# Kernel tuning notes

Hardware: AMD Instinct MI355X
Metric: run time of the kernel (lower is better)

The kernel has to match this reference:

```python
import jax, jax.numpy as jnp
import numpy as np

B, N, DIM = 16, 1024, 512
H, KD, D = 16, 32, 128          # num_heads, key_dim, d = attn_ratio*key_dim
DH = H * D                      # 2048
HQKV = DH + 2 * H * KD          # 3072
RES = 32
SCALE = KD ** -0.5
EPS = 1e-5


def _make_bias_idxs():
    ii = np.arange(N)
    px, py = ii // RES, ii % RES
    dx = np.abs(px[:, None] - px[None, :])
    dy = np.abs(py[:, None] - py[None, :])
    return (dx * RES + dy).astype(np.int32)  # (N, N), values in [0, RES*RES)


def setup_inputs() -> dict:
    key = jax.random.key(0)
    ks = jax.random.split(key, 6)
    return {
        "x": jax.random.normal(ks[0], (B, N, DIM), jnp.float32),
        "gamma": jnp.ones((DIM,), jnp.float32),
        "beta": jnp.zeros((DIM,), jnp.float32),
        "qkv_w": jax.random.normal(ks[1], (HQKV, DIM), jnp.float32) * 0.02,
        "qkv_b": jax.random.normal(ks[2], (HQKV,), jnp.float32) * 0.02,
        "proj_w": jax.random.normal(ks[3], (DIM, DH), jnp.float32) * 0.02,
        "proj_b": jax.random.normal(ks[4], (DIM,), jnp.float32) * 0.02,
        "attention_biases": jax.random.normal(ks[5], (H, RES * RES), jnp.float32) * 0.02,
        "bias_idxs": jnp.asarray(_make_bias_idxs()),
    }


def reference(x, gamma, beta, qkv_w, qkv_b, proj_w, proj_b, attention_biases, bias_idxs):
    # LayerNorm
    mu = jnp.mean(x, axis=-1, keepdims=True)
    var = jnp.mean(jnp.square(x - mu), axis=-1, keepdims=True)
    xn = (x - mu) * jax.lax.rsqrt(var + EPS) * gamma + beta
    # QKV projection -> (B, H, N, kd+kd+d)
    qkv = (xn @ qkv_w.T + qkv_b).reshape(B, N, H, 2 * KD + D).transpose(0, 2, 1, 3)
    q, k, v = qkv[..., :KD], qkv[..., KD:2 * KD], qkv[..., 2 * KD:]
    # Relative-position bias gather: (H, N, N)
    bias = attention_biases[:, bias_idxs]
    attn = jnp.einsum("bhnk,bhmk->bhnm", q, k) * SCALE + bias
    attn = jax.nn.softmax(attn, axis=-1)
    out = jnp.einsum("bhnm,bhmd->bhnd", attn, v)  # (B, H, N, D)
    out = out.transpose(0, 2, 1, 3).reshape(B, N, DH)
    return out @ proj_w.T + proj_b
```

## Files before the change

### kernel.cpp

```cpp
#include <hip/hip_runtime.h>

#define DIM_   512
#define NSEQ   1024
#define BB     16
#define HH     16
#define KD_    32
#define DD_    128
#define LDQKV  3072
#define DH_    2048
#define SCALE_ 0.17677669529663687f

typedef __bf16 bf16x8 __attribute__((ext_vector_type(8)));
typedef float  f32x4  __attribute__((ext_vector_type(4)));
typedef unsigned int u32x4v __attribute__((ext_vector_type(4)));

typedef __attribute__((address_space(1))) const unsigned int guint;
typedef __attribute__((address_space(3))) unsigned int luint;
#define GLL16(gp, lp) __builtin_amdgcn_global_load_lds((guint*)(gp), (luint*)(lp), 16, 0, 0)

static __device__ __forceinline__ unsigned short f2bf(float f) {
  unsigned int u = __builtin_bit_cast(unsigned int, f);
  u += 0x7fffu + ((u >> 16) & 1u);
  return (unsigned short)(u >> 16);
}
#define SGM(t) ((((t) & 3) << 1) | (((t) >> 2) & 1))

__global__ __launch_bounds__(256) void cvt_kernel(const float* __restrict__ in,
                                                  unsigned short* __restrict__ out,
                                                  int n) {
  int i = blockIdx.x * 256 + threadIdx.x;
  if (i < n) out[i] = f2bf(in[i]);
}

__global__ __launch_bounds__(256) void ln_kernel(const float* __restrict__ x,
                                                 const float* __restrict__ gamma,
                                                 const float* __restrict__ beta,
                                                 unsigned short* __restrict__ xn) {
  int row = blockIdx.x, t = threadIdx.x;
  const float* xr = x + (size_t)row * DIM_;
  float2 v = *(const float2*)(xr + t * 2);
  float s = v.x + v.y, sq = v.x * v.x + v.y * v.y;
#pragma unroll
  for (int off = 32; off; off >>= 1) {
    s  += __shfl_xor(s, off, 64);
    sq += __shfl_xor(sq, off, 64);
  }
  __shared__ float red[8];
  int wid = t >> 6, lane = t & 63;
  if (lane == 0) { red[wid * 2] = s; red[wid * 2 + 1] = sq; }
  __syncthreads();
  float S  = red[0] + red[2] + red[4] + red[6];
  float SQ = red[1] + red[3] + red[5] + red[7];
  float mu   = S * (1.f / DIM_);
  float var  = SQ * (1.f / DIM_) - mu * mu;
  float rstd = rsqrtf(var + 1e-5f);
  int c = t * 2;
  xn[(size_t)row * DIM_ + c]     = f2bf((v.x - mu) * rstd * gamma[c]     + beta[c]);
  xn[(size_t)row * DIM_ + c + 1] = f2bf((v.y - mu) * rstd * gamma[c + 1] + beta[c + 1]);
}

template <typename OUT>
__global__ __launch_bounds__(256) void gemm_gll(const unsigned short* __restrict__ A, int lda,
                                                const unsigned short* __restrict__ W, int ldb,
                                                const float* __restrict__ bias,
                                                OUT* __restrict__ C, int ldc,
                                                int K) {
  __shared__ unsigned short a_sm[128][64];
  __shared__ unsigned short b_sm[128][64];
  int tid = threadIdx.x;
  int lane = tid & 63, w = tid >> 6;
  int quad = lane >> 4, l15 = lane & 15;
  int wr = w >> 1, wc = w & 1;
  long tm = (long)blockIdx.y * 128, tn = (long)blockIdx.x * 128;
  int srow = w * 8 + (lane >> 3), scol = (lane & 7) * 8;

  f32x4 acc[4][4] = {};

  for (int k0 = 0; k0 < K; k0 += 64) {
    __syncthreads();
#pragma unroll
    for (int it = 0; it < 4; it++) {
      GLL16(A + (tm + it * 32 + srow) * lda + k0 + scol, &a_sm[it * 32 + w * 8][0]);
      GLL16(W + (tn + it * 32 + srow) * ldb + k0 + scol, &b_sm[it * 32 + w * 8][0]);
    }
    __syncthreads();
#pragma unroll
    for (int kk = 0; kk < 64; kk += 32) {
      bf16x8 af[4], bfr[4];
#pragma unroll
      for (int i = 0; i < 4; i++)
        af[i] = *(const bf16x8*)&a_sm[wr * 64 + i * 16 + l15][kk + quad * 8];
#pragma unroll
      for (int j = 0; j < 4; j++)
        bfr[j] = *(const bf16x8*)&b_sm[wc * 64 + j * 16 + l15][kk + quad * 8];
#pragma unroll
      for (int i = 0; i < 4; i++)
#pragma unroll
        for (int j = 0; j < 4; j++)
          acc[i][j] = __builtin_amdgcn_mfma_f32_16x16x32_bf16(af[i], bfr[j], acc[i][j], 0, 0, 0);
    }
  }
#pragma unroll
  for (int j = 0; j < 4; j++) {
    long col = tn + wc * 64 + j * 16 + l15;
    float bv = bias[col];
#pragma unroll
    for (int i = 0; i < 4; i++) {
      long row0 = tm + wr * 64 + i * 16 + quad * 4;
#pragma unroll
      for (int r = 0; r < 4; r++) {
        float val = acc[i][j][r] + bv;
        if constexpr (__is_same(OUT, float))
          C[(row0 + r) * ldc + col] = val;
        else
          C[(row0 + r) * ldc + col] = f2bf(val);
      }
    }
  }
}

__global__ __launch_bounds__(256) void attn_kernel(const unsigned short* __restrict__ qkv,
                                                   const float* __restrict__ ab,
                                                   unsigned short* __restrict__ attn_out) {
  __shared__ float lut[1024];
  __shared__ unsigned short vt[128][72];
  __shared__ unsigned short k_sm[64][40];

  int tid = threadIdx.x;
  int lane = tid & 63, w = tid >> 6;
  int quad = lane >> 4, l15 = lane & 15;

  int id = blockIdx.x;
  int bh = ((id >> 7) << 3) | (id & 7);
  int qb = (id >> 3) & 15;
  int b = bh >> 4, h = bh & 15;
  const unsigned short* base = qkv + (size_t)b * NSEQ * LDQKV + h * 192;

  for (int t = tid; t < 1024; t += 256) lut[t] = ab[h * 1024 + t];

  int qg = qb * 64 + w * 16 + l15;
  bf16x8 qf = *(const bf16x8*)(base + (size_t)qg * LDQKV + quad * 8);

  int rx = qg >> 5, ry = qg & 31;
  int dy_pre[8];
#pragma unroll
  for (int i = 0; i < 8; i++) {
    int cy = ((i >> 2) << 4) | (quad * 4 + (i & 3));
    int d = ry - cy; dy_pre[i] = d < 0 ? -d : d;
  }

  int ixA = ((quad & 1) * 32 + l15) * 4;
  int ixB = ixA + 64;
  bool hiq = quad >= 2;

  f32x4 accO[8] = {};
  float l_r = 0.f;

  int kkey = tid >> 2, kch = tid & 3;

  uint4 vreg[4];
  uint4 kreg;
#pragma unroll
  for (int i = 0; i < 4; i++) {
    int c = tid + i * 256;
    int m = c >> 4, c8 = c & 15;
    vreg[i] = *(const uint4*)(base + (size_t)m * LDQKV + 64 + c8 * 8);
  }
  kreg = *(const uint4*)(base + (size_t)kkey * LDQKV + 32 + kch * 8);

  for (int kt = 0; kt < 16; kt++) {
    __syncthreads();
#pragma unroll
    for (int i = 0; i < 4; i++) {
      int c = tid + i * 256;
      int m = c >> 4, c8 = c & 15;
      const unsigned short* pv = (const unsigned short*)&vreg[i];
      int col = (((m >> 3) ^ (c8 & 7)) << 3) | SGM(m & 7);
#pragma unroll
      for (int e = 0; e < 8; e++) vt[c8 * 8 + e][col] = pv[e];
    }
    *(uint4*)&k_sm[kkey][kch * 8] = kreg;
    __syncthreads();

    if (kt < 15) {
#pragma unroll
      for (int i = 0; i < 4; i++) {
        int c = tid + i * 256;
        int m = c >> 4, c8 = c & 15;
        vreg[i] = *(const uint4*)(base + (size_t)((kt + 1) * 64 + m) * LDQKV + 64 + c8 * 8);
      }
      kreg = *(const uint4*)(base + (size_t)((kt + 1) * 64 + kkey) * LDQKV + 32 + kch * 8);
    }

    f32x4 st[4];
#pragma unroll
    for (int nb = 0; nb < 4; nb++) {
      bf16x8 kf = *(const bf16x8*)&k_sm[nb * 16 + l15][quad * 8];
      f32x4 z = {};
      st[nb] = __builtin_amdgcn_mfma_f32_16x16x32_bf16(kf, qf, z, 0, 0, 0);
    }

    int d0 = rx - 2 * kt;     int dxa = d0 < 0 ? -d0 : d0;
    int d1 = d0 - 1;          int dxb = d1 < 0 ? -d1 : d1;
    int lb0 = dxa << 5, lb1 = dxb << 5;

    unsigned pk[8];
#pragma unroll
    for (int nb = 0; nb < 4; nb++) {
      int lb = (nb & 2) ? lb1 : lb0;
#pragma unroll
      for (int t = 0; t < 2; t++) {
        float p0 = __expf(fmaf(st[nb][2 * t],     SCALE_, lut[lb + dy_pre[(nb & 1) * 4 + 2 * t]]));
        float p1 = __expf(fmaf(st[nb][2 * t + 1], SCALE_, lut[lb + dy_pre[(nb & 1) * 4 + 2 * t + 1]]));
        l_r += p0 + p1;
        unsigned short u0 = __builtin_bit_cast(unsigned short, (__bf16)p0);
        unsigned short u1 = __builtin_bit_cast(unsigned short, (__bf16)p1);
        pk[nb * 2 + t] = (unsigned)u0 | ((unsigned)u1 << 16);
      }
    }

#pragma unroll
    for (int kc = 0; kc < 2; kc++) {
      int s0 = (int)pk[4 * kc + 0], s1 = (int)pk[4 * kc + 1];
      int s2 = (int)pk[4 * kc + 2], s3 = (int)pk[4 * kc + 3];
      unsigned a0 = (unsigned)__builtin_amdgcn_ds_bpermute(ixA, s0);
      unsigned a1 = (unsigned)__builtin_amdgcn_ds_bpermute(ixA, s1);
      unsigned a2 = (unsigned)__builtin_amdgcn_ds_bpermute(ixA, s2);
      unsigned a3 = (unsigned)__builtin_amdgcn_ds_bpermute(ixA, s3);
      unsigned b0 = (unsigned)__builtin_amdgcn_ds_bpermute(ixB, s0);
      unsigned b1 = (unsigned)__builtin_amdgcn_ds_bpermute(ixB, s1);
      unsigned b2 = (unsigned)__builtin_amdgcn_ds_bpermute(ixB, s2);
      unsigned b3 = (unsigned)__builtin_amdgcn_ds_bpermute(ixB, s3);
      unsigned u0 = hiq ? a2 : a0;
      unsigned u1 = hiq ? a3 : a1;
      unsigned v0 = hiq ? b2 : b0;
      unsigned v1 = hiq ? b3 : b1;
      u32x4v paw;
      paw.x = (u0 & 0xffffu) | (v0 << 16);
      paw.y = (u0 >> 16)     | (v0 & 0xffff0000u);
      paw.z = (u1 & 0xffffu) | (v1 << 16);
      paw.w = (u1 >> 16)     | (v1 & 0xffff0000u);
      bf16x8 paf = __builtin_bit_cast(bf16x8, paw);

#pragma unroll
      for (int db = 0; db < 8; db++) {
        int f = (db * 2 + (l15 >> 3)) & 7;
        int colb = ((kc * 4 + quad) ^ f) << 3;
        bf16x8 vf = *(const bf16x8*)&vt[db * 16 + l15][colb];
        accO[db] = __builtin_amdgcn_mfma_f32_16x16x32_bf16(paf, vf, accO[db], 0, 0, 0);
      }
    }
  }

  l_r += __shfl_xor(l_r, 16, 64);
  l_r += __shfl_xor(l_r, 32, 64);

#pragma unroll
  for (int r = 0; r < 4; r++) {
    float lr = __shfl(l_r, quad * 4 + r, 16);
    float inv = 1.f / lr;
    int row = qb * 64 + w * 16 + quad * 4 + r;
    size_t obase = ((size_t)b * NSEQ + row) * DH_ + h * DD_;
#pragma unroll
    for (int db = 0; db < 8; db++)
      attn_out[obase + db * 16 + l15] = f2bf(accO[db][r] * inv);
  }
}

extern "C" void kernel_launch(void* const* d_in, const int* in_sizes, int n_in,
                              void* d_out, int out_size, void* d_ws, size_t ws_size,
                              hipStream_t stream) {
  const float* x      = (const float*)d_in[0];
  const float* gamma  = (const float*)d_in[1];
  const float* beta   = (const float*)d_in[2];
  const float* qkv_w  = (const float*)d_in[3];
  const float* qkv_b  = (const float*)d_in[4];
  const float* proj_w = (const float*)d_in[5];
  const float* proj_b = (const float*)d_in[6];
  const float* ab     = (const float*)d_in[7];

  char* ws = (char*)d_ws;
  unsigned short* xn      = (unsigned short*)(ws);
  unsigned short* wqkv    = (unsigned short*)(ws + (size_t)16 * 1048576);
  unsigned short* wproj   = (unsigned short*)(ws + (size_t)19 * 1048576);
  unsigned short* qkv     = (unsigned short*)(ws + (size_t)21 * 1048576);
  unsigned short* attnout = (unsigned short*)(ws + (size_t)117 * 1048576);
  float* out = (float*)d_out;

  cvt_kernel<<<dim3(6144), dim3(256), 0, stream>>>(qkv_w, wqkv, 3072 * 512);
  cvt_kernel<<<dim3(4096), dim3(256), 0, stream>>>(proj_w, wproj, 512 * 2048);
  ln_kernel<<<dim3(16384), dim3(256), 0, stream>>>(x, gamma, beta, xn);
  gemm_gll<unsigned short><<<dim3(24, 128), dim3(256), 0, stream>>>(xn, 512, wqkv, 512, qkv_b, qkv, 3072, 512);
  attn_kernel<<<dim3(4096), dim3(256), 0, stream>>>(qkv, ab, attnout);
  gemm_gll<float><<<dim3(4, 128), dim3(256), 0, stream>>>(attnout, 2048, wproj, 2048, proj_b, out, 512, 2048);
}
```

Measured before the change: 491.2 us.

## Pre-transpose V into a global buffer and stream K/V into LDS asynchronously

Adds a transpose_v kernel that writes V per (batch, head) in a transposed, swizzled layout. The attention kernel can then fill its V and K tiles with direct global-to-LDS loads (global_load_lds) instead of staging them in registers and scattering them element by element into LDS. The attention output is written in place over the V slots of the qkv buffer, and the projection GEMM reads it back through a remapped A address, which removes the separate attnout buffer. The cost is an extra kernel launch and an extra pass over V. The register prefetch of the next tile is also dropped, so each iteration now waits on vmcnt(0) before computing.

New measurement: 449.5 us. 1.09x faster.

```diff
diff --git a/kernel.cpp b/kernel.cpp
--- a/kernel.cpp
+++ b/kernel.cpp
@@ -23,7 +23,6 @@
   u += 0x7fffu + ((u >> 16) & 1u);
   return (unsigned short)(u >> 16);
 }
-#define SGM(t) ((((t) & 3) << 1) | (((t) >> 2) & 1))
 
 __global__ __launch_bounds__(256) void cvt_kernel(const float* __restrict__ in,
                                                   unsigned short* __restrict__ out,
@@ -59,7 +58,7 @@
   xn[(size_t)row * DIM_ + c + 1] = f2bf((v.y - mu) * rstd * gamma[c + 1] + beta[c + 1]);
 }
 
-template <typename OUT>
+template <typename OUT, bool VREMAP>
 __global__ __launch_bounds__(256) void gemm_gll(const unsigned short* __restrict__ A, int lda,
                                                 const unsigned short* __restrict__ W, int ldb,
                                                 const float* __restrict__ bias,
@@ -80,7 +79,13 @@
     __syncthreads();
 #pragma unroll
     for (int it = 0; it < 4; it++) {
-      GLL16(A + (tm + it * 32 + srow) * lda + k0 + scol, &a_sm[it * 32 + w * 8][0]);
+      if constexpr (VREMAP) {
+        int kk = k0 + scol;
+        GLL16(A + (size_t)(tm + it * 32 + srow) * LDQKV + (kk >> 7) * 192 + 64 + (kk & 127),
+              &a_sm[it * 32 + w * 8][0]);
+      } else {
+        GLL16(A + (tm + it * 32 + srow) * lda + k0 + scol, &a_sm[it * 32 + w * 8][0]);
+      }
       GLL16(W + (tn + it * 32 + srow) * ldb + k0 + scol, &b_sm[it * 32 + w * 8][0]);
     }
     __syncthreads();
@@ -119,12 +124,41 @@
   }
 }
 
+__global__ __launch_bounds__(256) void transpose_v(const unsigned short* __restrict__ qkv,
+                                                   unsigned short* __restrict__ vT) {
+  __shared__ unsigned short lt[128][64];
+  int tid = threadIdx.x;
+  int nt = blockIdx.x, bh = blockIdx.y;
+  int b = bh >> 4, h = bh & 15;
+  const unsigned short* src = qkv + ((size_t)b * NSEQ + nt * 64) * LDQKV + h * 192 + 64;
+#pragma unroll
+  for (int i = 0; i < 4; i++) {
+    int u = tid + 256 * i;
+    int nl = u >> 4, d8 = u & 15;
+    uint4 r = *(const uint4*)(src + (size_t)nl * LDQKV + d8 * 8);
+    const unsigned short* pr = (const unsigned short*)&r;
+#pragma unroll
+    for (int e = 0; e < 8; e++)
+      lt[d8 * 8 + e][nl ^ ((d8 & 7) * 8)] = pr[e];
+  }
+  __syncthreads();
+  unsigned short* dst = vT + (size_t)bh * 131072 + nt * 64;
+#pragma unroll
+  for (int i = 0; i < 4; i++) {
+    int u = tid + 256 * i;
+    int d = u >> 3, p = u & 7;
+    int ct = p ^ ((d >> 3) & 7);
+    *(uint4*)(dst + (size_t)d * 1024 + ct * 8) = *(const uint4*)&lt[d][p * 8];
+  }
+}
+
 __global__ __launch_bounds__(256) void attn_kernel(const unsigned short* __restrict__ qkv,
+                                                   const unsigned short* __restrict__ vT,
                                                    const float* __restrict__ ab,
-                                                   unsigned short* __restrict__ attn_out) {
+                                                   unsigned short* attn_out) {
   __shared__ float lut[1024];
-  __shared__ unsigned short vt[128][72];
-  __shared__ unsigned short k_sm[64][40];
+  __shared__ unsigned short v_sm[128][64];
+  __shared__ unsigned short k_sm[64][32];
 
   int tid = threadIdx.x;
   int lane = tid & 63, w = tid >> 6;
@@ -135,6 +169,7 @@
   int qb = (id >> 3) & 15;
   int b = bh >> 4, h = bh & 15;
   const unsigned short* base = qkv + (size_t)b * NSEQ * LDQKV + h * 192;
+  const unsigned short* vTh = vT + (size_t)bh * 131072;
 
   for (int t = tid; t < 1024; t += 256) lut[t] = ab[h * 1024 + t];
 
@@ -156,41 +191,21 @@
   f32x4 accO[8] = {};
   float l_r = 0.f;
 
-  int kkey = tid >> 2, kch = tid & 3;
-
-  uint4 vreg[4];
-  uint4 kreg;
-#pragma unroll
-  for (int i = 0; i < 4; i++) {
-    int c = tid + i * 256;
-    int m = c >> 4, c8 = c & 15;
-    vreg[i] = *(const uint4*)(base + (size_t)m * LDQKV + 64 + c8 * 8);
-  }
-  kreg = *(const uint4*)(base + (size_t)kkey * LDQKV + 32 + kch * 8);
+  int vrow   = lane >> 3;
+  int vchunk = (lane & 7) ^ (lane >> 3);
+  int krow   = w * 16 + (lane >> 2);
+  int kcol   = (lane & 3) * 8;
 
   for (int kt = 0; kt < 16; kt++) {
     __syncthreads();
 #pragma unroll
     for (int i = 0; i < 4; i++) {
-      int c = tid + i * 256;
-      int m = c >> 4, c8 = c & 15;
-      const unsigned short* pv = (const unsigned short*)&vreg[i];
-      int col = (((m >> 3) ^ (c8 & 7)) << 3) | SGM(m & 7);
-#pragma unroll
-      for (int e = 0; e < 8; e++) vt[c8 * 8 + e][col] = pv[e];
-    }
-    *(uint4*)&k_sm[kkey][kch * 8] = kreg;
+      int r0 = (w * 4 + i) * 8;
+      GLL16(vTh + (size_t)(r0 + vrow) * 1024 + kt * 64 + vchunk * 8, &v_sm[r0][0]);
+    }
+    GLL16(base + (size_t)(kt * 64 + krow) * LDQKV + 32 + kcol, &k_sm[w * 16][0]);
+    asm volatile("s_waitcnt vmcnt(0)");
     __syncthreads();
-
-    if (kt < 15) {
-#pragma unroll
-      for (int i = 0; i < 4; i++) {
-        int c = tid + i * 256;
-        int m = c >> 4, c8 = c & 15;
-        vreg[i] = *(const uint4*)(base + (size_t)((kt + 1) * 64 + m) * LDQKV + 64 + c8 * 8);
-      }
-      kreg = *(const uint4*)(base + (size_t)((kt + 1) * 64 + kkey) * LDQKV + 32 + kch * 8);
-    }
 
     f32x4 st[4];
 #pragma unroll
@@ -231,22 +246,16 @@
       unsigned b1 = (unsigned)__builtin_amdgcn_ds_bpermute(ixB, s1);
       unsigned b2 = (unsigned)__builtin_amdgcn_ds_bpermute(ixB, s2);
       unsigned b3 = (unsigned)__builtin_amdgcn_ds_bpermute(ixB, s3);
-      unsigned u0 = hiq ? a2 : a0;
-      unsigned u1 = hiq ? a3 : a1;
-      unsigned v0 = hiq ? b2 : b0;
-      unsigned v1 = hiq ? b3 : b1;
       u32x4v paw;
-      paw.x = (u0 & 0xffffu) | (v0 << 16);
-      paw.y = (u0 >> 16)     | (v0 & 0xffff0000u);
-      paw.z = (u1 & 0xffffu) | (v1 << 16);
-      paw.w = (u1 >> 16)     | (v1 & 0xffff0000u);
+      paw.x = hiq ? a2 : a0;
+      paw.y = hiq ? a3 : a1;
+      paw.z = hiq ? b2 : b0;
+      paw.w = hiq ? b3 : b1;
       bf16x8 paf = __builtin_bit_cast(bf16x8, paw);
 
 #pragma unroll
       for (int db = 0; db < 8; db++) {
-        int f = (db * 2 + (l15 >> 3)) & 7;
-        int colb = ((kc * 4 + quad) ^ f) << 3;
-        bf16x8 vf = *(const bf16x8*)&vt[db * 16 + l15][colb];
+        bf16x8 vf = *(const bf16x8*)&v_sm[db * 16 + l15][((kc * 4 + quad) ^ (l15 & 7)) * 8];
         accO[db] = __builtin_amdgcn_mfma_f32_16x16x32_bf16(paf, vf, accO[db], 0, 0, 0);
       }
     }
@@ -260,7 +269,7 @@
     float lr = __shfl(l_r, quad * 4 + r, 16);
     float inv = 1.f / lr;
     int row = qb * 64 + w * 16 + quad * 4 + r;
-    size_t obase = ((size_t)b * NSEQ + row) * DH_ + h * DD_;
+    size_t obase = ((size_t)b * NSEQ + row) * LDQKV + h * 192 + 64;
 #pragma unroll
     for (int db = 0; db < 8; db++)
       attn_out[obase + db * 16 + l15] = f2bf(accO[db][r] * inv);
@@ -280,17 +289,18 @@
   const float* ab     = (const float*)d_in[7];
 
   char* ws = (char*)d_ws;
-  unsigned short* xn      = (unsigned short*)(ws);
-  unsigned short* wqkv    = (unsigned short*)(ws + (size_t)16 * 1048576);
-  unsigned short* wproj   = (unsigned short*)(ws + (size_t)19 * 1048576);
-  unsigned short* qkv     = (unsigned short*)(ws + (size_t)21 * 1048576);
-  unsigned short* attnout = (unsigned short*)(ws + (size_t)117 * 1048576);
+  unsigned short* xn    = (unsigned short*)(ws);
+  unsigned short* wqkv  = (unsigned short*)(ws + (size_t)16 * 1048576);
+  unsigned short* wproj = (unsigned short*)(ws + (size_t)19 * 1048576);
+  unsigned short* qkv   = (unsigned short*)(ws + (size_t)21 * 1048576);
+  unsigned short* vT    = (unsigned short*)(ws + (size_t)117 * 1048576);
   float* out = (float*)d_out;
 
   cvt_kernel<<<dim3(6144), dim3(256), 0, stream>>>(qkv_w, wqkv, 3072 * 512);
   cvt_kernel<<<dim3(4096), dim3(256), 0, stream>>>(proj_w, wproj, 512 * 2048);
   ln_kernel<<<dim3(16384), dim3(256), 0, stream>>>(x, gamma, beta, xn);
-  gemm_gll<unsigned short><<<dim3(24, 128), dim3(256), 0, stream>>>(xn, 512, wqkv, 512, qkv_b, qkv, 3072, 512);
-  attn_kernel<<<dim3(4096), dim3(256), 0, stream>>>(qkv, ab, attnout);
-  gemm_gll<float><<<dim3(4, 128), dim3(256), 0, stream>>>(attnout, 2048, wproj, 2048, proj_b, out, 512, 2048);
-}
+  gemm_gll<unsigned short, false><<<dim3(24, 128), dim3(256), 0, stream>>>(xn, 512, wqkv, 512, qkv_b, qkv, 3072, 512);
+  transpose_v<<<dim3(16, 256), dim3(256), 0, stream>>>(qkv, vT);
+  attn_kernel<<<dim3(4096), dim3(256), 0, stream>>>(qkv, vT, ab, qkv);
+  gemm_gll<float, true><<<dim3(4, 128), dim3(256), 0, stream>>>(qkv, 3072, wproj, 2048, proj_b, out, 512, 2048);
+}
```
